# Kernel optimization log

Measured on AMD Instinct MI355X. Metric: run time of the kernel, lower is better.

## Reference

```python
import jax, jax.numpy as jnp
import numpy as np


def setup_inputs() -> dict:
    key = jax.random.key(0)
    k1, k2, k3, k4, k5 = jax.random.split(key, 5)
    B, S, K, N, G = 4, 2048, 4096, 4096, 64  # G = group_size -> num_groups = K // G = 64
    x = jax.random.normal(k1, (B, S, K), dtype=jnp.float32)
    # int2 codes stored one-per-int8 slot (low 2 bits valid); use int32 container
    weight_q = jax.random.randint(k2, (N, K), 0, 4, dtype=jnp.int32)
    scale = jax.random.uniform(k3, (N, K // G), dtype=jnp.float32) * 0.05 + 0.01
    zp = jax.random.uniform(k4, (N, K // G), dtype=jnp.float32) * 3.0
    bias = jax.random.normal(k5, (N,), dtype=jnp.float32)
    return {"x": x, "weight_q": weight_q, "scale": scale, "zp": zp, "bias": bias}


def _dequant(weight_q, scale, zp):
    # weight_q: [N, K] int codes in [0,4); scale/zp: [N, num_groups]
    N, K = weight_q.shape
    num_groups = scale.shape[1]
    gs = K // num_groups  # group_size
    q = weight_q.astype(jnp.float32).reshape(N, num_groups, gs)
    w = (q - zp[:, :, None]) * scale[:, :, None]
    return w.reshape(N, K)


def reference(x, weight_q, scale, zp, bias):
    # asymm_qw2_gemm: out = x @ dequant(W)^T + bias
    w = _dequant(weight_q, scale, zp)            # [N, K]
    out = jnp.einsum('bsk,nk->bsn', x, w)        # [B, S, N]
    return out + bias
```

## Files before the change

### kernel.cpp

```cpp
#include <hip/hip_runtime.h>
#include <stdint.h>


typedef __attribute__((ext_vector_type(4))) float  f32x4;
typedef __attribute__((ext_vector_type(4))) int    i32x4;
typedef __attribute__((ext_vector_type(8))) __bf16 bf16x8;
typedef __attribute__((ext_vector_type(8))) unsigned short u16x8;

__device__ __forceinline__ unsigned short f2bf(float f) {
  unsigned u = __builtin_bit_cast(unsigned, f);
  u += 0x7fffu + ((u >> 16) & 1u);
  return (unsigned short)(u >> 16);
}

__device__ __forceinline__ void async16(const void* g, void* l) {
  __builtin_amdgcn_global_load_lds(
      (const __attribute__((address_space(1))) unsigned int*)g,
      (__attribute__((address_space(3))) unsigned int*)l, 16, 0, 0);
}

__global__ __launch_bounds__(256) void prep_kernel(
    const float* __restrict__ x, unsigned short* __restrict__ xb, int xunits,
    const int* __restrict__ wq, const float* __restrict__ scale,
    const float* __restrict__ zp, unsigned short* __restrict__ wb,
    int wunits, int K, int G, int ng) {
  const int stride = gridDim.x * 256;
  const int i0 = blockIdx.x * 256 + threadIdx.x;
  for (int u = i0; u < xunits; u += stride) {
    const f32x4* xp = (const f32x4*)x + (size_t)u * 2;
    f32x4 a = xp[0], b = xp[1];
    u16x8 o;
    o[0] = f2bf(a[0]); o[1] = f2bf(a[1]); o[2] = f2bf(a[2]); o[3] = f2bf(a[3]);
    o[4] = f2bf(b[0]); o[5] = f2bf(b[1]); o[6] = f2bf(b[2]); o[7] = f2bf(b[3]);
    *((u16x8*)xb + u) = o;
  }
  for (int u = i0; u < wunits; u += stride) {
    int k8 = u * 8;
    int n = k8 / K, kk = k8 % K;
    int g = kk / G;
    float s  = scale[(size_t)n * ng + g];
    float bz = -zp[(size_t)n * ng + g] * s;
    const i32x4* wp = (const i32x4*)wq + (size_t)u * 2;
    i32x4 qa = wp[0], qb = wp[1];
    u16x8 o;
    o[0] = f2bf((float)qa[0] * s + bz); o[1] = f2bf((float)qa[1] * s + bz);
    o[2] = f2bf((float)qa[2] * s + bz); o[3] = f2bf((float)qa[3] * s + bz);
    o[4] = f2bf((float)qb[0] * s + bz); o[5] = f2bf((float)qb[1] * s + bz);
    o[6] = f2bf((float)qb[2] * s + bz); o[7] = f2bf((float)qb[3] * s + bz);
    *((u16x8*)wb + u) = o;
  }
}

#define BM 256
#define BN 256
#define TK 64
#define RSZ (128 * 64)

__global__ __launch_bounds__(512, 2) void gemm_bt_kernel(
    const unsigned short* __restrict__ A,
    const unsigned short* __restrict__ B,
    const float* __restrict__ bias,
    float* __restrict__ C, int M, int N, int K) {
  __shared__ unsigned short As[4 * RSZ];
  __shared__ unsigned short Bs[4 * RSZ];

  const int tid  = threadIdx.x;
  const int lane = tid & 63;
  const int wave = tid >> 6;
  const int wm = wave >> 2, wn = wave & 3;
  const int q = lane >> 4, r = lane & 15;

  int id = blockIdx.x;
  {
    int nwg = gridDim.x;
    if ((nwg & 7) == 0) id = (id & 7) * (nwg >> 3) + (id >> 3);
  }
  const int nbx = N / BN;
  const int m0 = (id / nbx) * BM;
  const int n0 = (id % nbx) * BN;

  const int wgA = wave & 3;
  const int bh  = wn >> 1;
  const int wgB = (wave & 1) | ((wave >> 2) << 1);
  const int lr8 = lane >> 3;
  const int gc  = (lane & 7) ^ (lr8 & 7);
  const unsigned short* aGbase =
      A + (size_t)(m0 + wm * 128 + wgA * 32 + lr8) * K + gc * 8;
  const unsigned short* bGbase =
      B + (size_t)(n0 + bh * 128 + wgB * 32 + lr8) * K + gc * 8;

#define STG_A(np, kk) { \
    unsigned short* d = As + ((np) * 2 + wm) * RSZ + wgA * 2048 + (lane << 3); \
    const unsigned short* g = aGbase + (kk); \
    async16(g,                  d);        \
    async16(g +  8 * (size_t)K, d +  512); \
    async16(g + 16 * (size_t)K, d + 1024); \
    async16(g + 24 * (size_t)K, d + 1536); }

#define STG_B(np, kk) { \
    unsigned short* d = Bs + ((np) * 2 + bh) * RSZ + wgB * 2048 + (lane << 3); \
    const unsigned short* g = bGbase + (kk); \
    async16(g,                  d);        \
    async16(g +  8 * (size_t)K, d +  512); \
    async16(g + 16 * (size_t)K, d + 1024); \
    async16(g + 24 * (size_t)K, d + 1536); }

  const int key  = r & 7;
  const int cho0 = ((q) ^ key) * 8;
  const int cho1 = ((4 + q) ^ key) * 8;
  const int aoff0 = r * 64 + cho0, aoff1 = r * 64 + cho1;
  const int boff0 = ((wn & 1) * 64 + r) * 64 + cho0;
  const int boff1 = ((wn & 1) * 64 + r) * 64 + cho1;

  f32x4 acc[8][4] = {};
  const int NT = K / TK;

  STG_A(0, 0) STG_B(0, 0)
  asm volatile("s_waitcnt vmcnt(0)" ::: "memory");
  __builtin_amdgcn_s_barrier();
  asm volatile("" ::: "memory");

#pragma unroll 1
  for (int t = 0; t < NT; ++t) {
    const int par = t & 1, np = par ^ 1;
    const bool pf = (t + 1 < NT);
    const int kk1 = (t + 1) * TK;
    const unsigned short* Ar = As + (par * 2 + wm) * RSZ;
    const unsigned short* Br = Bs + (par * 2 + bh) * RSZ;

    bf16x8 bb0[4], bb1[4];

    {
      bf16x8 aa0[2], aa1[2];
#pragma unroll
      for (int nj = 0; nj < 4; ++nj) {
        bb0[nj] = *(const bf16x8*)&Br[nj * 1024 + boff0];
        bb1[nj] = *(const bf16x8*)&Br[nj * 1024 + boff1];
      }
#pragma unroll
      for (int m2 = 0; m2 < 2; ++m2) {
        aa0[m2] = *(const bf16x8*)&Ar[m2 * 1024 + aoff0];
        aa1[m2] = *(const bf16x8*)&Ar[m2 * 1024 + aoff1];
      }
      if (pf) STG_A(np, kk1)
      asm volatile("s_waitcnt lgkmcnt(8)" ::: "memory");
      __builtin_amdgcn_s_barrier();
      asm volatile("s_waitcnt lgkmcnt(0)" ::: "memory");
      __builtin_amdgcn_s_setprio(1);
#pragma unroll
      for (int m2 = 0; m2 < 2; ++m2)
#pragma unroll
        for (int nj = 0; nj < 4; ++nj) {
          acc[m2][nj] = __builtin_amdgcn_mfma_f32_16x16x32_bf16(
              aa0[m2], bb0[nj], acc[m2][nj], 0, 0, 0);
          acc[m2][nj] = __builtin_amdgcn_mfma_f32_16x16x32_bf16(
              aa1[m2], bb1[nj], acc[m2][nj], 0, 0, 0);
        }
      __builtin_amdgcn_s_setprio(0);
      asm volatile("" ::: "memory");
      __builtin_amdgcn_s_barrier();
      asm volatile("" ::: "memory");
    }

#pragma unroll
    for (int p = 1; p < 4; ++p) {
      bf16x8 aa0[2], aa1[2];
#pragma unroll
      for (int m2 = 0; m2 < 2; ++m2) {
        aa0[m2] = *(const bf16x8*)&Ar[(2 * p + m2) * 1024 + aoff0];
        aa1[m2] = *(const bf16x8*)&Ar[(2 * p + m2) * 1024 + aoff1];
      }
      if (p == 1 && pf) STG_B(np, kk1)
      __builtin_amdgcn_s_barrier();
      asm volatile("s_waitcnt lgkmcnt(0)" ::: "memory");
      __builtin_amdgcn_s_setprio(1);
#pragma unroll
      for (int m2 = 0; m2 < 2; ++m2)
#pragma unroll
        for (int nj = 0; nj < 4; ++nj) {
          acc[2 * p + m2][nj] = __builtin_amdgcn_mfma_f32_16x16x32_bf16(
              aa0[m2], bb0[nj], acc[2 * p + m2][nj], 0, 0, 0);
          acc[2 * p + m2][nj] = __builtin_amdgcn_mfma_f32_16x16x32_bf16(
              aa1[m2], bb1[nj], acc[2 * p + m2][nj], 0, 0, 0);
        }
      __builtin_amdgcn_s_setprio(0);
      asm volatile("" ::: "memory");
      if (p == 3) asm volatile("s_waitcnt vmcnt(0)" ::: "memory");
      __builtin_amdgcn_s_barrier();
      asm volatile("" ::: "memory");
    }
  }

  float bv[4];
#pragma unroll
  for (int j = 0; j < 4; ++j) bv[j] = bias[n0 + wn * 64 + j * 16 + r];
#pragma unroll
  for (int i = 0; i < 8; ++i) {
    int mbase = m0 + wm * 128 + i * 16 + q * 4;
#pragma unroll
    for (int e = 0; e < 4; ++e) {
      float* crow = C + (size_t)(mbase + e) * N + n0 + wn * 64 + r;
#pragma unroll
      for (int j = 0; j < 4; ++j)
        crow[j * 16] = acc[i][j][e] + bv[j];
    }
  }
}

__global__ __launch_bounds__(256) void naive_kernel(
    const float* __restrict__ x, const int* __restrict__ wq,
    const float* __restrict__ scale, const float* __restrict__ zp,
    const float* __restrict__ bias, float* __restrict__ out,
    int M, int N, int K, int G) {
  int idx = blockIdx.x * 256 + threadIdx.x;
  if (idx >= M * N) return;
  int m = idx / N, n = idx % N;
  const float* xr = x + (size_t)m * K;
  const int* wr = wq + (size_t)n * K;
  int ng = K / G;
  float acc = 0.f;
  for (int g = 0; g < ng; ++g) {
    float s = scale[(size_t)n * ng + g];
    float b = -zp[(size_t)n * ng + g] * s;
    for (int k = 0; k < G; ++k)
      acc += xr[g * G + k] * ((float)wr[g * G + k] * s + b);
  }
  out[idx] = acc + bias[n];
}

extern "C" void kernel_launch(void* const* d_in, const int* in_sizes, int n_in,
                              void* d_out, int out_size, void* d_ws, size_t ws_size,
                              hipStream_t stream) {
  const float* x     = (const float*)d_in[0];
  const int*   wq    = (const int*)d_in[1];
  const float* scale = (const float*)d_in[2];
  const float* zp    = (const float*)d_in[3];
  const float* bias  = (const float*)d_in[4];
  float* out = (float*)d_out;

  const int N  = in_sizes[4];
  const int K  = in_sizes[1] / N;
  const int ng = in_sizes[2] / N;
  const int G  = K / ng;
  const int M  = in_sizes[0] / K;

  size_t xb_bytes = (size_t)M * K * 2;
  size_t wb_bytes = (size_t)N * K * 2;
  bool divisible = (M % BM == 0) && (N % BN == 0) && (K % TK == 0) &&
                   (G % 8 == 0);
  if (ws_size < xb_bytes + wb_bytes || !divisible) {
    int total = M * N;
    naive_kernel<<<dim3((total + 255) / 256), dim3(256), 0, stream>>>(
        x, wq, scale, zp, bias, out, M, N, K, G);
    return;
  }

  unsigned short* xb = (unsigned short*)d_ws;
  unsigned short* wb = (unsigned short*)((char*)d_ws + xb_bytes);

  int xunits = M * K / 8;
  int wunits = N * K / 8;
  prep_kernel<<<dim3(2048), dim3(256), 0, stream>>>(
      x, xb, xunits, wq, scale, zp, wb, wunits, K, G, ng);

  dim3 grid((M / BM) * (N / BN));
  gemm_bt_kernel<<<grid, dim3(512), 0, stream>>>(xb, wb, bias, out, M, N, K);
}
```

Measured before the change: 531.5 us.

## Switch GEMM main loop to 4-stage LDS ring with TK=32

Halves the K-tile depth to 32 and replaces the double-buffered LDS pipeline with a four-slot ring that keeps three tiles of global-to-LDS loads in flight. It uses a new simplified staging and swizzle layout and graded vmcnt waits. The goal is to hide global memory latency better with deeper prefetch. In exchange there are more loop iterations and barriers per K and fewer MFMAs per barrier phase, and the new swizzle could still cause LDS bank conflicts.

```diff
diff --git a/kernel.cpp b/kernel.cpp
--- a/kernel.cpp
+++ b/kernel.cpp
@@ -53,8 +53,8 @@
 
 #define BM 256
 #define BN 256
-#define TK 64
-#define RSZ (128 * 64)
+#define TK 32
+#define RSZ (256 * 32)
 
 __global__ __launch_bounds__(512, 2) void gemm_bt_kernel(
     const unsigned short* __restrict__ A,
@@ -79,116 +79,91 @@
   const int m0 = (id / nbx) * BM;
   const int n0 = (id % nbx) * BN;
 
-  const int wgA = wave & 3;
-  const int bh  = wn >> 1;
-  const int wgB = (wave & 1) | ((wave >> 2) << 1);
-  const int lr8 = lane >> 3;
-  const int gc  = (lane & 7) ^ (lr8 & 7);
-  const unsigned short* aGbase =
-      A + (size_t)(m0 + wm * 128 + wgA * 32 + lr8) * K + gc * 8;
-  const unsigned short* bGbase =
-      B + (size_t)(n0 + bh * 128 + wgB * 32 + lr8) * K + gc * 8;
-
-#define STG_A(np, kk) { \
-    unsigned short* d = As + ((np) * 2 + wm) * RSZ + wgA * 2048 + (lane << 3); \
-    const unsigned short* g = aGbase + (kk); \
-    async16(g,                  d);        \
-    async16(g +  8 * (size_t)K, d +  512); \
-    async16(g + 16 * (size_t)K, d + 1024); \
-    async16(g + 24 * (size_t)K, d + 1536); }
-
-#define STG_B(np, kk) { \
-    unsigned short* d = Bs + ((np) * 2 + bh) * RSZ + wgB * 2048 + (lane << 3); \
-    const unsigned short* g = bGbase + (kk); \
-    async16(g,                  d);        \
-    async16(g +  8 * (size_t)K, d +  512); \
-    async16(g + 16 * (size_t)K, d + 1024); \
-    async16(g + 24 * (size_t)K, d + 1536); }
-
-  const int key  = r & 7;
-  const int cho0 = ((q) ^ key) * 8;
-  const int cho1 = ((4 + q) ^ key) * 8;
-  const int aoff0 = r * 64 + cho0, aoff1 = r * 64 + cho1;
-  const int boff0 = ((wn & 1) * 64 + r) * 64 + cho0;
-  const int boff1 = ((wn & 1) * 64 + r) * 64 + cho1;
+  const int srow = tid >> 2;
+  const int gch  = (tid & 3) ^ ((tid >> 3) & 3);
+  const unsigned short* aG = A + (size_t)(m0 + srow) * K + gch * 8;
+  const unsigned short* bG = B + (size_t)(n0 + srow) * K + gch * 8;
+  const size_t rb = (size_t)128 * K;
+
+  unsigned short* aS = As + tid * 8;
+  unsigned short* bS = Bs + tid * 8;
+
+#define STG_A(slot, kk) { \
+    unsigned short* d = aS + (slot) * RSZ; \
+    async16(aG + (kk), d); async16(aG + rb + (kk), d + 4096); }
+#define STG_B(slot, kk) { \
+    unsigned short* d = bS + (slot) * RSZ; \
+    async16(bG + (kk), d); async16(bG + rb + (kk), d + 4096); }
+
+  const int qc8  = ((q ^ ((r >> 1) & 3))) * 8;
+  const int aoff = (wm * 128 + r) * 32 + qc8;
+  const int boff = (wn * 64  + r) * 32 + qc8;
 
   f32x4 acc[8][4] = {};
   const int NT = K / TK;
 
   STG_A(0, 0) STG_B(0, 0)
-  asm volatile("s_waitcnt vmcnt(0)" ::: "memory");
+  if (NT > 1) { STG_A(1, TK) STG_B(1, TK) }
+  if (NT > 2) { STG_A(2, 2 * TK) STG_B(2, 2 * TK) }
+  if (NT > 2)      asm volatile("s_waitcnt vmcnt(8)" ::: "memory");
+  else if (NT > 1) asm volatile("s_waitcnt vmcnt(4)" ::: "memory");
+  else             asm volatile("s_waitcnt vmcnt(0)" ::: "memory");
   __builtin_amdgcn_s_barrier();
   asm volatile("" ::: "memory");
 
 #pragma unroll 1
   for (int t = 0; t < NT; ++t) {
-    const int par = t & 1, np = par ^ 1;
-    const bool pf = (t + 1 < NT);
-    const int kk1 = (t + 1) * TK;
-    const unsigned short* Ar = As + (par * 2 + wm) * RSZ;
-    const unsigned short* Br = Bs + (par * 2 + bh) * RSZ;
-
-    bf16x8 bb0[4], bb1[4];
-
+    const int slot = t & 3;
+    const bool pf = (t + 3 < NT);
+    const unsigned short* Ar = As + slot * RSZ;
+    const unsigned short* Br = Bs + slot * RSZ;
+
+    bf16x8 bf[4], af[4];
+
+#pragma unroll
+    for (int nj = 0; nj < 4; ++nj)
+      bf[nj] = *(const bf16x8*)&Br[boff + nj * 512];
+#pragma unroll
+    for (int mi = 0; mi < 4; ++mi)
+      af[mi] = *(const bf16x8*)&Ar[aoff + mi * 512];
+    if (pf) STG_A((t + 3) & 3, (t + 3) * TK)
+    __builtin_amdgcn_s_barrier();
+    asm volatile("s_waitcnt lgkmcnt(0)" ::: "memory");
+    __builtin_amdgcn_s_setprio(1);
+#pragma unroll
+    for (int mi = 0; mi < 4; ++mi)
+#pragma unroll
+      for (int nj = 0; nj < 4; ++nj)
+        acc[mi][nj] = __builtin_amdgcn_mfma_f32_16x16x32_bf16(
+            af[mi], bf[nj], acc[mi][nj], 0, 0, 0);
+    __builtin_amdgcn_s_setprio(0);
+    asm volatile("" ::: "memory");
+    __builtin_amdgcn_s_barrier();
+    asm volatile("" ::: "memory");
+
+#pragma unroll
+    for (int mi = 0; mi < 4; ++mi)
+      af[mi] = *(const bf16x8*)&Ar[aoff + (4 + mi) * 512];
+    if (pf) STG_B((t + 3) & 3, (t + 3) * TK)
     {
-      bf16x8 aa0[2], aa1[2];
-#pragma unroll
-      for (int nj = 0; nj < 4; ++nj) {
-        bb0[nj] = *(const bf16x8*)&Br[nj * 1024 + boff0];
-        bb1[nj] = *(const bf16x8*)&Br[nj * 1024 + boff1];
-      }
-#pragma unroll
-      for (int m2 = 0; m2 < 2; ++m2) {
-        aa0[m2] = *(const bf16x8*)&Ar[m2 * 1024 + aoff0];
-        aa1[m2] = *(const bf16x8*)&Ar[m2 * 1024 + aoff1];
-      }
-      if (pf) STG_A(np, kk1)
-      asm volatile("s_waitcnt lgkmcnt(8)" ::: "memory");
-      __builtin_amdgcn_s_barrier();
-      asm volatile("s_waitcnt lgkmcnt(0)" ::: "memory");
-      __builtin_amdgcn_s_setprio(1);
-#pragma unroll
-      for (int m2 = 0; m2 < 2; ++m2)
-#pragma unroll
-        for (int nj = 0; nj < 4; ++nj) {
-          acc[m2][nj] = __builtin_amdgcn_mfma_f32_16x16x32_bf16(
-              aa0[m2], bb0[nj], acc[m2][nj], 0, 0, 0);
-          acc[m2][nj] = __builtin_amdgcn_mfma_f32_16x16x32_bf16(
-              aa1[m2], bb1[nj], acc[m2][nj], 0, 0, 0);
-        }
-      __builtin_amdgcn_s_setprio(0);
-      asm volatile("" ::: "memory");
-      __builtin_amdgcn_s_barrier();
-      asm volatile("" ::: "memory");
+      int rem = ((t + 3 < NT ? t + 3 : NT - 1)) - (t + 1);
+      if (rem >= 2)      asm volatile("s_waitcnt vmcnt(8)" ::: "memory");
+      else if (rem == 1) asm volatile("s_waitcnt vmcnt(4)" ::: "memory");
+      else               asm volatile("s_waitcnt vmcnt(0)" ::: "memory");
     }
-
-#pragma unroll
-    for (int p = 1; p < 4; ++p) {
-      bf16x8 aa0[2], aa1[2];
-#pragma unroll
-      for (int m2 = 0; m2 < 2; ++m2) {
-        aa0[m2] = *(const bf16x8*)&Ar[(2 * p + m2) * 1024 + aoff0];
-        aa1[m2] = *(const bf16x8*)&Ar[(2 * p + m2) * 1024 + aoff1];
-      }
-      if (p == 1 && pf) STG_B(np, kk1)
-      __builtin_amdgcn_s_barrier();
-      asm volatile("s_waitcnt lgkmcnt(0)" ::: "memory");
-      __builtin_amdgcn_s_setprio(1);
-#pragma unroll
-      for (int m2 = 0; m2 < 2; ++m2)
-#pragma unroll
-        for (int nj = 0; nj < 4; ++nj) {
-          acc[2 * p + m2][nj] = __builtin_amdgcn_mfma_f32_16x16x32_bf16(
-              aa0[m2], bb0[nj], acc[2 * p + m2][nj], 0, 0, 0);
-          acc[2 * p + m2][nj] = __builtin_amdgcn_mfma_f32_16x16x32_bf16(
-              aa1[m2], bb1[nj], acc[2 * p + m2][nj], 0, 0, 0);
-        }
-      __builtin_amdgcn_s_setprio(0);
-      asm volatile("" ::: "memory");
-      if (p == 3) asm volatile("s_waitcnt vmcnt(0)" ::: "memory");
-      __builtin_amdgcn_s_barrier();
-      asm volatile("" ::: "memory");
-    }
+    __builtin_amdgcn_s_barrier();
+    asm volatile("s_waitcnt lgkmcnt(0)" ::: "memory");
+    __builtin_amdgcn_s_setprio(1);
+#pragma unroll
+    for (int mi = 0; mi < 4; ++mi)
+#pragma unroll
+      for (int nj = 0; nj < 4; ++nj)
+        acc[4 + mi][nj] = __builtin_amdgcn_mfma_f32_16x16x32_bf16(
+            af[mi], bf[nj], acc[4 + mi][nj], 0, 0, 0);
+    __builtin_amdgcn_s_setprio(0);
+    asm volatile("" ::: "memory");
+    __builtin_amdgcn_s_barrier();
+    asm volatile("" ::: "memory");
   }
 
   float bv[4];
```

After: 558.4 us. 5.1% more time.
